# Kernel tuning notes

Hardware: AMD Instinct MI355X
Metric: run time of the kernel (lower is better)

## Reference

```python
import jax, jax.numpy as jnp
import numpy as np

B, S, E, H = 4, 2048, 512, 1024

def setup_inputs() -> dict:
    key = jax.random.key(0)
    ks = jax.random.split(key, 8)
    s = 1.0 / np.sqrt(H)
    return {
        "hidden_states": jax.random.normal(ks[0], (B, S, H), jnp.float32),
        "external_embeddings": jax.random.normal(ks[1], (B, E, H), jnp.float32),
        "Wq": jax.random.normal(ks[2], (H, H), jnp.float32) * s,
        "bq": jax.random.normal(ks[3], (H,), jnp.float32) * 0.02,
        "Wk": jax.random.normal(ks[4], (H, H), jnp.float32) * s,
        "bk": jax.random.normal(ks[5], (H,), jnp.float32) * 0.02,
        "Wv": jax.random.normal(ks[6], (H, H), jnp.float32) * s,
        "bv": jax.random.normal(ks[7], (H,), jnp.float32) * 0.02,
    }

def reference(hidden_states, external_embeddings, Wq, bq, Wk, bk, Wv, bv):
    # Projections (torch Linear semantics: here weights stored as [in,out])
    q = hidden_states @ Wq + bq              # [B,S,H]
    k_tok = hidden_states @ Wk + bk          # [B,S,H]
    v_tok = hidden_states @ Wv + bv          # [B,S,H]
    k_ext = external_embeddings @ Wk + bk    # [B,E,H]
    v_ext = external_embeddings @ Wv + bv    # [B,E,H]
    # Each token attends to [its own key] ++ [external keys]; NO 1/sqrt(d) scaling
    # and NO head splitting, matching the original forward exactly.
    s_self = jnp.einsum('bsh,bsh->bs', q, k_tok)[..., None]   # [B,S,1]
    s_ext = jnp.einsum('bsh,beh->bse', q, k_ext)              # [B,S,E]
    scores = jnp.concatenate([s_self, s_ext], axis=-1)        # [B,S,1+E]
    probs = jax.nn.softmax(scores, axis=-1)
    ctx = probs[..., :1] * v_tok + jnp.einsum('bse,beh->bsh', probs[..., 1:], v_ext)
    return ctx  # [B,S,H]
```

## Files before the change

kernel.cpp:

```cpp
#include <hip/hip_runtime.h>
#include <stdint.h>

#define BB 4
#define SS 2048
#define EE 512
#define HH 1024

typedef _Float16 f16;
typedef __attribute__((ext_vector_type(8))) _Float16 f16x8;
typedef __attribute__((ext_vector_type(4))) _Float16 f16x4;
typedef __attribute__((ext_vector_type(4))) float f32x4;

__device__ __forceinline__ void async16(void* lds, const void* g) {
  __builtin_amdgcn_global_load_lds(
      (const __attribute__((address_space(1))) unsigned int*)g,
      (__attribute__((address_space(3))) unsigned int*)lds, 16, 0, 0);
}

#define MFMA16 __builtin_amdgcn_mfma_f32_16x16x32_f16

template <int TERMS>
__device__ __forceinline__ void gemm_core(
    const f16* Ah, const f16* Al, const f16* Bh, const f16* Bl, int K, int ld,
    f16* lAh, f16* lAl, f16* lBh, f16* lBl, f32x4 acc[4][4]) {
  const int tid = threadIdx.x;
  const int wave = tid >> 6;
  const int lane = tid & 63;
  const int lrow = lane >> 2;
  const int lcol = (((lane & 3) ^ ((lane >> 3) & 3))) * 8;
  const int waveM = (wave >> 1) * 64;
  const int waveN = (wave & 1) * 64;
  const int frow = lane & 15;
  const int fk = ((lane >> 4) ^ ((frow >> 1) & 3)) * 8;

  for (int k0 = 0; k0 < K; k0 += 32) {
    __syncthreads();
#pragma unroll
    for (int i = 0; i < 2; ++i) {
      const int r0 = (wave * 2 + i) * 16;
      const size_t goff = (size_t)(r0 + lrow) * ld + (k0 + lcol);
      async16(&lAh[r0 * 32], Ah + goff);
      async16(&lBh[r0 * 32], Bh + goff);
      if (TERMS >= 2) async16(&lBl[r0 * 32], Bl + goff);
      if (TERMS >= 3) async16(&lAl[r0 * 32], Al + goff);
    }
    __syncthreads();

    f16x8 a[4], bh[4], bl[4], al[4];
#pragma unroll
    for (int i = 0; i < 4; ++i) {
      a[i] = *(const f16x8*)&lAh[(waveM + i * 16 + frow) * 32 + fk];
      bh[i] = *(const f16x8*)&lBh[(waveN + i * 16 + frow) * 32 + fk];
      if (TERMS >= 2) bl[i] = *(const f16x8*)&lBl[(waveN + i * 16 + frow) * 32 + fk];
      if (TERMS >= 3) al[i] = *(const f16x8*)&lAl[(waveM + i * 16 + frow) * 32 + fk];
    }
#pragma unroll
    for (int i = 0; i < 4; ++i)
#pragma unroll
      for (int j = 0; j < 4; ++j) {
        acc[i][j] = MFMA16(a[i], bh[j], acc[i][j], 0, 0, 0);
        if (TERMS >= 2)
          acc[i][j] = MFMA16(a[i], bl[j], acc[i][j], 0, 0, 0);
        if (TERMS >= 3)
          acc[i][j] = MFMA16(al[i], bh[j], acc[i][j], 0, 0, 0);
      }
  }
}

__global__ __launch_bounds__(256) void cast_kernel(const float* __restrict__ xh32,
                                                   const float* __restrict__ xe32,
                                                   f16* __restrict__ xh,
                                                   f16* __restrict__ xe) {
  const int i = blockIdx.x * 256 + threadIdx.x;
  const int n4h = 8192 * HH / 4;
  const float* src = i < n4h ? xh32 : xe32;
  f16* dst = i < n4h ? xh : xe;
  const int k = i < n4h ? i : i - n4h;
  const float4 v = ((const float4*)src)[k];
  f16x4 o;
  o.x = (f16)v.x; o.y = (f16)v.y; o.z = (f16)v.z; o.w = (f16)v.w;
  ((f16x4*)dst)[k] = o;
}

__global__ void wsplit_kernel(const float* __restrict__ Wq, const float* __restrict__ Wk,
                              const float* __restrict__ Wv, f16* __restrict__ wt_hi,
                              f16* __restrict__ wt_lo) {
  __shared__ float tile[32][33];
  const int k0 = blockIdx.x * 32;
  const int n0g = blockIdx.y * 32;
  const int which = n0g >> 10;
  const float* W = which == 0 ? Wq : (which == 1 ? Wk : Wv);
  const int n0 = n0g & 1023;
  const int tx = threadIdx.x, ty = threadIdx.y;
#pragma unroll
  for (int i = 0; i < 32; i += 8)
    tile[ty + i][tx] = W[(size_t)(k0 + ty + i) * 1024 + n0 + tx];
  __syncthreads();
#pragma unroll
  for (int i = 0; i < 32; i += 8) {
    const int np = n0g + ty + i;
    const float v = tile[tx][ty + i];
    const size_t idx = (size_t)np * 1024 + k0 + tx;
    const f16 h = (f16)v;
    wt_hi[idx] = h;
    wt_lo[idx] = (f16)(v - (float)h);
  }
}

__global__ __launch_bounds__(512, 2) void proj_kernel(
    const f16* __restrict__ xh, const f16* __restrict__ xe,
    const f16* __restrict__ wt_hi, const f16* __restrict__ wt_lo,
    const float* __restrict__ bq, const float* __restrict__ bk,
    const float* __restrict__ bv, f16* __restrict__ q_hi, f16* __restrict__ q_lo,
    f16* __restrict__ kt, f16* __restrict__ vt,
    f16* __restrict__ ke_hi, f16* __restrict__ ke_lo, f16* __restrict__ veT) {
  const int g = blockIdx.x;
  const int j = g & 7;
  const int s = g >> 3;
  int mrow0, colB0;
  bool ext = false, splitB = false;
  if (s < 20) {
    splitB = true;
    if (s < 16) {
      colB0 = (s >> 2) * 256;
      mrow0 = ((s & 3) * 8 + j) * 256;
    } else {
      ext = true;
      colB0 = 1024 + (s - 16) * 256;
      mrow0 = j * 256;
    }
  } else {
    const int s2 = s - 20;
    if (s2 < 32) {
      colB0 = (4 + (s2 >> 2)) * 256;
      mrow0 = ((s2 & 3) * 8 + j) * 256;
    } else {
      ext = true;
      colB0 = 1024 + (4 + (s2 - 32)) * 256;
      mrow0 = j * 256;
    }
  }
  const int NT = splitB ? 32 : 16;

  __shared__ f16 lds[65536];

  const int tid = threadIdx.x;
  const int wave = tid >> 6, lane = tid & 63;
  const int wm = wave >> 2, wn = wave & 3;
  const int frow = lane & 15, qd = lane >> 4;

  const f16* A0 = (ext ? xe : xh) + (size_t)mrow0 * HH;
  const f16* Bhi = wt_hi + (size_t)colB0 * HH;
  const f16* Blo = wt_lo + (size_t)colB0 * HH;

  const int srow = tid >> 2;
  const int scol = ((tid & 3) ^ ((srow >> 1) & 3)) * 8;
  const size_t gO0 = (size_t)srow * HH + scol;
  const size_t gO1 = (size_t)(128 + srow) * HH + scol;
  const int ldst0 = (wave * 64) * 8;
  const int ldst1 = (512 + wave * 64) * 8;

  int offA[8], offB[4];
#pragma unroll
  for (int i = 0; i < 8; ++i) {
    const int r = wm * 128 + i * 16 + frow;
    offA[i] = r * 32 + ((qd ^ ((r >> 1) & 3)) * 8);
  }
#pragma unroll
  for (int jj = 0; jj < 4; ++jj) {
    const int r = wn * 64 + jj * 16 + frow;
    offB[jj] = r * 32 + ((qd ^ ((r >> 1) & 3)) * 8);
  }

  f32x4 acc[8][4];
#pragma unroll
  for (int i = 0; i < 8; ++i)
#pragma unroll
    for (int jj = 0; jj < 4; ++jj)
#pragma unroll
      for (int r = 0; r < 4; ++r) acc[i][jj][r] = 0.0f;

  {
    f16* dA0 = &lds[0];
    f16* dB0 = &lds[32768];
    f16* dA1 = &lds[8192];
    f16* dB1 = &lds[32768 + 8192];
    async16(&dA0[ldst0], A0 + gO0);       async16(&dA0[ldst1], A0 + gO1);
    async16(&dB0[ldst0], Bhi + gO0);      async16(&dB0[ldst1], Bhi + gO1);
    async16(&dA1[ldst0], A0 + 32 + gO0);  async16(&dA1[ldst1], A0 + 32 + gO1);
    async16(&dB1[ldst0], Bhi + 32 + gO0); async16(&dB1[ldst1], Bhi + 32 + gO1);
  }
  asm volatile("s_waitcnt vmcnt(4)" ::: "memory");
  __builtin_amdgcn_s_barrier();

  for (int t = 0; t < NT; ++t) {
    const int cur = t & 1, nxt = cur ^ 1;
    const bool st = (t + 1 < NT);
    const int kn = ((t + 1) & 15) * 64;
    const f16* An = A0 + kn;
    const f16* Bn = (((t + 1) & 16) ? Blo : Bhi) + kn;
    const f16* lA0 = &lds[(cur * 2 + 0) * 8192];
    const f16* lB0 = &lds[32768 + (cur * 2 + 0) * 8192];
    const f16* lA1 = &lds[(cur * 2 + 1) * 8192];
    const f16* lB1 = &lds[32768 + (cur * 2 + 1) * 8192];
    f16* sA0 = &lds[(nxt * 2 + 0) * 8192];
    f16* sB0 = &lds[32768 + (nxt * 2 + 0) * 8192];
    f16* sA1 = &lds[(nxt * 2 + 1) * 8192];
    f16* sB1 = &lds[32768 + (nxt * 2 + 1) * 8192];

    f16x8 a[8], b0, b1;

#pragma unroll
    for (int i = 0; i < 8; ++i) a[i] = *(const f16x8*)&lA0[offA[i]];
    b0 = *(const f16x8*)&lB0[offB[0]];
    b1 = *(const f16x8*)&lB0[offB[1]];
    if (st) { async16(&sA0[ldst0], An + gO0); async16(&sA0[ldst1], An + gO1); }
    __builtin_amdgcn_s_barrier();
    __builtin_amdgcn_s_setprio(1);
#pragma unroll
    for (int i = 0; i < 8; ++i) {
      acc[i][0] = MFMA16(a[i], b0, acc[i][0], 0, 0, 0);
      acc[i][1] = MFMA16(a[i], b1, acc[i][1], 0, 0, 0);
    }
    __builtin_amdgcn_s_setprio(0);
    __builtin_amdgcn_s_barrier();

    b0 = *(const f16x8*)&lB0[offB[2]];
    b1 = *(const f16x8*)&lB0[offB[3]];
    if (st) { async16(&sB0[ldst0], Bn + gO0); async16(&sB0[ldst1], Bn + gO1); }
    __builtin_amdgcn_s_barrier();
    __builtin_amdgcn_s_setprio(1);
#pragma unroll
    for (int i = 0; i < 8; ++i) {
      acc[i][2] = MFMA16(a[i], b0, acc[i][2], 0, 0, 0);
      acc[i][3] = MFMA16(a[i], b1, acc[i][3], 0, 0, 0);
    }
    __builtin_amdgcn_s_setprio(0);
    if (t == NT - 1) {
      asm volatile("s_waitcnt vmcnt(0)" ::: "memory");
    } else {
      asm volatile("s_waitcnt vmcnt(4)" ::: "memory");
    }
    __builtin_amdgcn_s_barrier();

#pragma unroll
    for (int i = 0; i < 8; ++i) a[i] = *(const f16x8*)&lA1[offA[i]];
    b0 = *(const f16x8*)&lB1[offB[0]];
    b1 = *(const f16x8*)&lB1[offB[1]];
    if (st) { async16(&sA1[ldst0], An + 32 + gO0); async16(&sA1[ldst1], An + 32 + gO1); }
    __builtin_amdgcn_s_barrier();
    __builtin_amdgcn_s_setprio(1);
#pragma unroll
    for (int i = 0; i < 8; ++i) {
      acc[i][0] = MFMA16(a[i], b0, acc[i][0], 0, 0, 0);
      acc[i][1] = MFMA16(a[i], b1, acc[i][1], 0, 0, 0);
    }
    __builtin_amdgcn_s_setprio(0);
    __builtin_amdgcn_s_barrier();

    b0 = *(const f16x8*)&lB1[offB[2]];
    b1 = *(const f16x8*)&lB1[offB[3]];
    if (st) { async16(&sB1[ldst0], Bn + 32 + gO0); async16(&sB1[ldst1], Bn + 32 + gO1); }
    __builtin_amdgcn_s_barrier();
    __builtin_amdgcn_s_setprio(1);
#pragma unroll
    for (int i = 0; i < 8; ++i) {
      acc[i][2] = MFMA16(a[i], b0, acc[i][2], 0, 0, 0);
      acc[i][3] = MFMA16(a[i], b1, acc[i][3], 0, 0, 0);
    }
    __builtin_amdgcn_s_setprio(0);
    asm volatile("s_waitcnt vmcnt(4)" ::: "memory");
    __builtin_amdgcn_s_barrier();
  }

  const int er0 = wm * 128 + qd * 4;
  const int ec0 = wn * 64 + frow;
  float bias[4];
#pragma unroll
  for (int jj = 0; jj < 4; ++jj) {
    const int c = colB0 + ec0 + jj * 16;
    bias[jj] = c < 1024 ? bq[c] : (c < 2048 ? bk[c - 1024] : bv[c - 2048]);
  }

  if (!ext) {
    if (colB0 < 1024) {
#pragma unroll
      for (int jj = 0; jj < 4; ++jj) {
        const int c = colB0 + ec0 + jj * 16;
#pragma unroll
        for (int i = 0; i < 8; ++i)
#pragma unroll
          for (int r = 0; r < 4; ++r) {
            const int row = mrow0 + er0 + i * 16 + r;
            const float val = acc[i][jj][r] + bias[jj];
            const size_t idx = (size_t)row * HH + c;
            const f16 h = (f16)val;
            q_hi[idx] = h;
            q_lo[idx] = (f16)(val - (float)h);
          }
      }
    } else if (colB0 < 2048) {
#pragma unroll
      for (int jj = 0; jj < 4; ++jj) {
        const int c = colB0 + ec0 + jj * 16 - 1024;
#pragma unroll
        for (int i = 0; i < 8; ++i)
#pragma unroll
          for (int r = 0; r < 4; ++r) {
            const int row = mrow0 + er0 + i * 16 + r;
            kt[(size_t)row * HH + c] = (f16)(acc[i][jj][r] + bias[jj]);
          }
      }
    } else {
#pragma unroll
      for (int jj = 0; jj < 4; ++jj) {
        const int c = colB0 + ec0 + jj * 16 - 2048;
#pragma unroll
        for (int i = 0; i < 8; ++i)
#pragma unroll
          for (int r = 0; r < 4; ++r) {
            const int row = mrow0 + er0 + i * 16 + r;
            vt[(size_t)row * HH + c] = (f16)(acc[i][jj][r] + bias[jj]);
          }
      }
    }
  } else {
    if (colB0 < 2048) {
#pragma unroll
      for (int jj = 0; jj < 4; ++jj) {
        const int c = colB0 + ec0 + jj * 16 - 1024;
#pragma unroll
        for (int i = 0; i < 8; ++i)
#pragma unroll
          for (int r = 0; r < 4; ++r) {
            const int row = mrow0 + er0 + i * 16 + r;
            const float val = acc[i][jj][r] + bias[jj];
            const size_t idx = (size_t)row * HH + c;
            const f16 h = (f16)val;
            ke_hi[idx] = h;
            ke_lo[idx] = (f16)(val - (float)h);
          }
      }
    } else {
      f16* tl = lds;
      const int b = mrow0 >> 9, e0 = mrow0 & 511;
      const int h0 = colB0 - 2048;
#pragma unroll
      for (int p = 0; p < 2; ++p) {
        __syncthreads();
        if ((wn >> 1) == p) {
          const int hL = (wn & 1) * 64 + frow;
#pragma unroll
          for (int jj = 0; jj < 4; ++jj)
#pragma unroll
            for (int i = 0; i < 8; ++i)
#pragma unroll
              for (int r = 0; r < 4; ++r) {
                const int e = er0 + i * 16 + r;
                tl[(hL + jj * 16) * 264 + e] = (f16)(acc[i][jj][r] + bias[jj]);
              }
        }
        __syncthreads();
        for (int c = tid; c < 128 * 32; c += 512) {
          const int hL = c >> 5, ch = c & 31;
          const f16x8 v = *(const f16x8*)&tl[hL * 264 + ch * 8];
          *(f16x8*)&veT[(size_t)(b * HH + h0 + p * 128 + hL) * EE + e0 + ch * 8] = v;
        }
      }
    }
  }
}

__global__ __launch_bounds__(256, 4) void score_kernel(
    const f16* __restrict__ q_hi, const f16* __restrict__ q_lo,
    const f16* __restrict__ ke_hi, const f16* __restrict__ ke_lo,
    float* __restrict__ s_part) {
  const int b = blockIdx.z & 3;
  const int khalf = blockIdx.z >> 2;
  const int mtile = blockIdx.y;
  const int ntile = blockIdx.x;
  __shared__ f16 lds[4 * 4096];
  const size_t aoff = ((size_t)b * SS + mtile * 128) * HH + khalf * 512;
  const size_t boff = ((size_t)b * EE + ntile * 128) * HH + khalf * 512;

  f32x4 acc[4][4];
#pragma unroll
  for (int i = 0; i < 4; ++i)
#pragma unroll
    for (int j = 0; j < 4; ++j)
#pragma unroll
      for (int r = 0; r < 4; ++r) acc[i][j][r] = 0.0f;

  gemm_core<3>(q_hi + aoff, q_lo + aoff, ke_hi + boff, ke_lo + boff, 512, HH,
               lds, lds + 4096, lds + 8192, lds + 12288, acc);

  float* dst = s_part + (size_t)khalf * BB * SS * EE;
  const int tid = threadIdx.x, wave = tid >> 6, lane = tid & 63;
  const int waveM = (wave >> 1) * 64, waveN = (wave & 1) * 64;
  const int colIn16 = lane & 15, rowQuad = (lane >> 4) * 4;
#pragma unroll
  for (int j = 0; j < 4; ++j) {
    const int e = ntile * 128 + waveN + j * 16 + colIn16;
#pragma unroll
    for (int i = 0; i < 4; ++i)
#pragma unroll
      for (int r = 0; r < 4; ++r) {
        const int s = mtile * 128 + waveM + i * 16 + rowQuad + r;
        dst[((size_t)b * SS + s) * EE + e] = acc[i][j][r];
      }
  }
}

__global__ __launch_bounds__(256) void softmax_kernel(
    const f16* __restrict__ q_hi, const f16* __restrict__ q_lo,
    const f16* __restrict__ kt, const float* __restrict__ s_part,
    f16* __restrict__ probs, float* __restrict__ p_self) {
  const int t = blockIdx.x * 4 + (threadIdx.x >> 6);
  const int lane = threadIdx.x & 63;

  const size_t base = (size_t)t * HH;
  float ss = 0.f;
#pragma unroll
  for (int it = 0; it < 4; ++it) {
    const int off = it * 256 + lane * 4;
    const f16x4 qh = *(const f16x4*)&q_hi[base + off];
    const f16x4 ql = *(const f16x4*)&q_lo[base + off];
    const f16x4 kh = *(const f16x4*)&kt[base + off];
    ss += ((float)qh.x + (float)ql.x) * (float)kh.x;
    ss += ((float)qh.y + (float)ql.y) * (float)kh.y;
    ss += ((float)qh.z + (float)ql.z) * (float)kh.z;
    ss += ((float)qh.w + (float)ql.w) * (float)kh.w;
  }
#pragma unroll
  for (int m = 32; m > 0; m >>= 1) ss += __shfl_xor(ss, m, 64);

  const float* r0 = s_part + (size_t)t * EE;
  const float* r1 = s_part + (size_t)BB * SS * EE + (size_t)t * EE;
  const float4 a0 = *(const float4*)&r0[lane * 4];
  const float4 a1 = *(const float4*)&r0[256 + lane * 4];
  const float4 c0 = *(const float4*)&r1[lane * 4];
  const float4 c1 = *(const float4*)&r1[256 + lane * 4];
  const float v0x = a0.x + c0.x, v0y = a0.y + c0.y, v0z = a0.z + c0.z, v0w = a0.w + c0.w;
  const float v1x = a1.x + c1.x, v1y = a1.y + c1.y, v1z = a1.z + c1.z, v1w = a1.w + c1.w;
  float m = fmaxf(fmaxf(fmaxf(v0x, v0y), fmaxf(v0z, v0w)),
                  fmaxf(fmaxf(v1x, v1y), fmaxf(v1z, v1w)));
#pragma unroll
  for (int sh = 32; sh > 0; sh >>= 1) m = fmaxf(m, __shfl_xor(m, sh, 64));
  m = fmaxf(m, ss);
  const float e0 = __expf(v0x - m), e1 = __expf(v0y - m);
  const float e2 = __expf(v0z - m), e3 = __expf(v0w - m);
  const float e4 = __expf(v1x - m), e5 = __expf(v1y - m);
  const float e6 = __expf(v1z - m), e7 = __expf(v1w - m);
  float sum = ((e0 + e1) + (e2 + e3)) + ((e4 + e5) + (e6 + e7));
#pragma unroll
  for (int sh = 32; sh > 0; sh >>= 1) sum += __shfl_xor(sum, sh, 64);
  const float es = __expf(ss - m);
  const float inv = 1.0f / (sum + es);
  f16x4 p0, p1;
  p0.x = (f16)(e0 * inv); p0.y = (f16)(e1 * inv);
  p0.z = (f16)(e2 * inv); p0.w = (f16)(e3 * inv);
  p1.x = (f16)(e4 * inv); p1.y = (f16)(e5 * inv);
  p1.z = (f16)(e6 * inv); p1.w = (f16)(e7 * inv);
  *(f16x4*)&probs[(size_t)t * EE + lane * 4] = p0;
  *(f16x4*)&probs[(size_t)t * EE + 256 + lane * 4] = p1;
  if (lane == 0) p_self[t] = es * inv;
}

__global__ __launch_bounds__(256, 4) void pv_kernel(
    const f16* __restrict__ probs, const f16* __restrict__ veT,
    const float* __restrict__ p_self, const f16* __restrict__ vt,
    float* __restrict__ out) {
  const int b = blockIdx.z;
  const int mtile = blockIdx.y;
  const int ntile = blockIdx.x;
  __shared__ f16 lds[2 * 4096];
  const size_t aoff = ((size_t)b * SS + mtile * 128) * EE;
  const size_t boff = ((size_t)b * HH + ntile * 128) * EE;

  f32x4 acc[4][4];
#pragma unroll
  for (int i = 0; i < 4; ++i)
#pragma unroll
    for (int j = 0; j < 4; ++j)
#pragma unroll
      for (int r = 0; r < 4; ++r) acc[i][j][r] = 0.0f;

  gemm_core<1>(probs + aoff, nullptr, veT + boff, nullptr, EE, EE,
               lds, nullptr, lds + 4096, nullptr, acc);

  const int tid = threadIdx.x, wave = tid >> 6, lane = tid & 63;
  const int waveM = (wave >> 1) * 64, waveN = (wave & 1) * 64;
  const int colIn16 = lane & 15, rowQuad = (lane >> 4) * 4;
#pragma unroll
  for (int j = 0; j < 4; ++j) {
    const int h = ntile * 128 + waveN + j * 16 + colIn16;
#pragma unroll
    for (int i = 0; i < 4; ++i)
#pragma unroll
      for (int r = 0; r < 4; ++r) {
        const int s = mtile * 128 + waveM + i * 16 + rowQuad + r;
        const size_t t = (size_t)b * SS + s;
        __builtin_nontemporal_store(
            acc[i][j][r] + p_self[t] * (float)vt[t * HH + h], &out[t * HH + h]);
      }
  }
}

extern "C" void kernel_launch(void* const* d_in, const int* in_sizes, int n_in,
                              void* d_out, int out_size, void* d_ws, size_t ws_size,
                              hipStream_t stream) {
  const float* hidden = (const float*)d_in[0];
  const float* ext    = (const float*)d_in[1];
  const float* Wq = (const float*)d_in[2];
  const float* bq = (const float*)d_in[3];
  const float* Wk = (const float*)d_in[4];
  const float* bk = (const float*)d_in[5];
  const float* Wv = (const float*)d_in[6];
  const float* bv = (const float*)d_in[7];
  float* out = (float*)d_out;

  char* ws = (char*)d_ws;
  size_t off = 0;
  auto alloc = [&](size_t bytes) {
    char* p = ws + off;
    off += (bytes + 255) & ~(size_t)255;
    return p;
  };
  const size_t TOK = 8192, EXT = 2048;
  f16* xh    = (f16*)alloc(TOK * HH * 2);
  f16* xe    = (f16*)alloc(EXT * HH * 2);
  f16* wt_hi = (f16*)alloc(3072ull * HH * 2);
  f16* wt_lo = (f16*)alloc(3072ull * HH * 2);
  f16* q_hi  = (f16*)alloc(TOK * HH * 2);
  f16* q_lo  = (f16*)alloc(TOK * HH * 2);
  f16* kt    = (f16*)alloc(TOK * HH * 2);
  f16* vt    = (f16*)alloc(TOK * HH * 2);
  f16* ke_hi = (f16*)alloc(EXT * HH * 2);
  f16* ke_lo = (f16*)alloc(EXT * HH * 2);
  f16* veT   = (f16*)alloc((size_t)BB * HH * EE * 2);
  float* p_self = (float*)alloc(TOK * 4);
  float* s_part = (float*)alloc(2ull * BB * SS * EE * 4);
  f16* probs    = (f16*)alloc((size_t)BB * SS * EE * 2);

  cast_kernel<<<10240, 256, 0, stream>>>(hidden, ext, xh, xe);
  wsplit_kernel<<<dim3(32, 96), dim3(32, 8), 0, stream>>>(Wq, Wk, Wv, wt_hi, wt_lo);

  proj_kernel<<<448, 512, 0, stream>>>(
      xh, xe, wt_hi, wt_lo, bq, bk, bv,
      q_hi, q_lo, kt, vt, ke_hi, ke_lo, veT);

  score_kernel<<<dim3(4, 16, 8), 256, 0, stream>>>(q_hi, q_lo, ke_hi, ke_lo, s_part);
  softmax_kernel<<<2048, 256, 0, stream>>>(q_hi, q_lo, kt, s_part, probs, p_self);
  pv_kernel<<<dim3(8, 16, 4), 256, 0, stream>>>(probs, veT, p_self, vt, out);
}
```

Measured before the change: 306.1 us.

## Pipeline score and PV GEMMs with multi-buffered LDS and larger 256-row tiles

Replaces the shared single-buffered gemm_core in score_kernel and pv_kernel with custom pipelines. Score uses double-buffered LDS and pv uses triple-buffered LDS, with async global-to-LDS loads for the next K slice interleaved between MFMA phases under explicit vmcnt waits and s_setprio. Blocks grow to 512 threads covering 256x128 output tiles, so each B tile is reused across more rows. The goal is to hide load latency behind MFMA work and cut barrier stalls, at the cost of more LDS per block, fewer blocks, and fragile hand-counted wait counts.

```diff
diff --git a/kernel.cpp b/kernel.cpp
--- a/kernel.cpp
+++ b/kernel.cpp
@@ -18,54 +18,6 @@
 }
 
 #define MFMA16 __builtin_amdgcn_mfma_f32_16x16x32_f16
-
-template <int TERMS>
-__device__ __forceinline__ void gemm_core(
-    const f16* Ah, const f16* Al, const f16* Bh, const f16* Bl, int K, int ld,
-    f16* lAh, f16* lAl, f16* lBh, f16* lBl, f32x4 acc[4][4]) {
-  const int tid = threadIdx.x;
-  const int wave = tid >> 6;
-  const int lane = tid & 63;
-  const int lrow = lane >> 2;
-  const int lcol = (((lane & 3) ^ ((lane >> 3) & 3))) * 8;
-  const int waveM = (wave >> 1) * 64;
-  const int waveN = (wave & 1) * 64;
-  const int frow = lane & 15;
-  const int fk = ((lane >> 4) ^ ((frow >> 1) & 3)) * 8;
-
-  for (int k0 = 0; k0 < K; k0 += 32) {
-    __syncthreads();
-#pragma unroll
-    for (int i = 0; i < 2; ++i) {
-      const int r0 = (wave * 2 + i) * 16;
-      const size_t goff = (size_t)(r0 + lrow) * ld + (k0 + lcol);
-      async16(&lAh[r0 * 32], Ah + goff);
-      async16(&lBh[r0 * 32], Bh + goff);
-      if (TERMS >= 2) async16(&lBl[r0 * 32], Bl + goff);
-      if (TERMS >= 3) async16(&lAl[r0 * 32], Al + goff);
-    }
-    __syncthreads();
-
-    f16x8 a[4], bh[4], bl[4], al[4];
-#pragma unroll
-    for (int i = 0; i < 4; ++i) {
-      a[i] = *(const f16x8*)&lAh[(waveM + i * 16 + frow) * 32 + fk];
-      bh[i] = *(const f16x8*)&lBh[(waveN + i * 16 + frow) * 32 + fk];
-      if (TERMS >= 2) bl[i] = *(const f16x8*)&lBl[(waveN + i * 16 + frow) * 32 + fk];
-      if (TERMS >= 3) al[i] = *(const f16x8*)&lAl[(waveM + i * 16 + frow) * 32 + fk];
-    }
-#pragma unroll
-    for (int i = 0; i < 4; ++i)
-#pragma unroll
-      for (int j = 0; j < 4; ++j) {
-        acc[i][j] = MFMA16(a[i], bh[j], acc[i][j], 0, 0, 0);
-        if (TERMS >= 2)
-          acc[i][j] = MFMA16(a[i], bl[j], acc[i][j], 0, 0, 0);
-        if (TERMS >= 3)
-          acc[i][j] = MFMA16(al[i], bh[j], acc[i][j], 0, 0, 0);
-      }
-  }
-}
 
 __global__ __launch_bounds__(256) void cast_kernel(const float* __restrict__ xh32,
                                                    const float* __restrict__ xe32,
@@ -371,7 +323,7 @@
   }
 }
 
-__global__ __launch_bounds__(256, 4) void score_kernel(
+__global__ __launch_bounds__(512, 2) void score_kernel(
     const f16* __restrict__ q_hi, const f16* __restrict__ q_lo,
     const f16* __restrict__ ke_hi, const f16* __restrict__ ke_lo,
     float* __restrict__ s_part) {
@@ -379,34 +331,137 @@
   const int khalf = blockIdx.z >> 2;
   const int mtile = blockIdx.y;
   const int ntile = blockIdx.x;
-  __shared__ f16 lds[4 * 4096];
-  const size_t aoff = ((size_t)b * SS + mtile * 128) * HH + khalf * 512;
+
+  __shared__ f16 lds[49152];
+
+  const int tid = threadIdx.x;
+  const int wave = tid >> 6, lane = tid & 63;
+  const int wm = wave >> 1, wn = wave & 1;
+  const int frow = lane & 15, qd = lane >> 4;
+
+  const size_t aoff = ((size_t)b * SS + mtile * 256) * HH + khalf * 512;
   const size_t boff = ((size_t)b * EE + ntile * 128) * HH + khalf * 512;
+  const f16* Ah = q_hi + aoff;
+  const f16* Al = q_lo + aoff;
+  const f16* Bh = ke_hi + boff;
+  const f16* Bl = ke_lo + boff;
+
+  const int srow = tid >> 2;
+  const int scol = ((tid & 3) ^ ((srow >> 1) & 3)) * 8;
+  const size_t gA0 = (size_t)srow * HH + scol;
+  const size_t gA1 = (size_t)(128 + srow) * HH + scol;
+  const int ldstA0 = (wave * 64) * 8;
+  const int ldstA1 = (512 + wave * 64) * 8;
+  const int ldstB0 = (wave * 64) * 8;
+
+  int offA[4], offB[4];
+#pragma unroll
+  for (int i = 0; i < 4; ++i) {
+    const int r = wm * 64 + i * 16 + frow;
+    offA[i] = r * 32 + ((qd ^ ((r >> 1) & 3)) * 8);
+  }
+#pragma unroll
+  for (int jj = 0; jj < 4; ++jj) {
+    const int r = wn * 64 + jj * 16 + frow;
+    offB[jj] = r * 32 + ((qd ^ ((r >> 1) & 3)) * 8);
+  }
 
   f32x4 acc[4][4];
 #pragma unroll
   for (int i = 0; i < 4; ++i)
 #pragma unroll
-    for (int j = 0; j < 4; ++j)
-#pragma unroll
-      for (int r = 0; r < 4; ++r) acc[i][j][r] = 0.0f;
-
-  gemm_core<3>(q_hi + aoff, q_lo + aoff, ke_hi + boff, ke_lo + boff, 512, HH,
-               lds, lds + 4096, lds + 8192, lds + 12288, acc);
-
-  float* dst = s_part + (size_t)khalf * BB * SS * EE;
-  const int tid = threadIdx.x, wave = tid >> 6, lane = tid & 63;
-  const int waveM = (wave >> 1) * 64, waveN = (wave & 1) * 64;
-  const int colIn16 = lane & 15, rowQuad = (lane >> 4) * 4;
-#pragma unroll
-  for (int j = 0; j < 4; ++j) {
-    const int e = ntile * 128 + waveN + j * 16 + colIn16;
+    for (int jj = 0; jj < 4; ++jj)
+#pragma unroll
+      for (int r = 0; r < 4; ++r) acc[i][jj][r] = 0.0f;
+
+  {
+    f16* dAh = &lds[0];
+    f16* dAl = &lds[8192];
+    f16* dBh = &lds[16384];
+    f16* dBl = &lds[20480];
+    async16(&dAh[ldstA0], Ah + gA0); async16(&dAh[ldstA1], Ah + gA1);
+    async16(&dBh[ldstB0], Bh + gA0);
+    async16(&dBl[ldstB0], Bl + gA0);
+    async16(&dAl[ldstA0], Al + gA0); async16(&dAl[ldstA1], Al + gA1);
+  }
+  asm volatile("s_waitcnt vmcnt(3)" ::: "memory");
+  __builtin_amdgcn_s_barrier();
+
+  for (int t = 0; t < 16; ++t) {
+    const int cur = t & 1, nxt = cur ^ 1;
+    const bool st = (t < 15);
+    const int kk = (t + 1) * 32;
+    const f16* lAh = &lds[cur * 24576];
+    const f16* lAl = &lds[cur * 24576 + 8192];
+    const f16* lBh = &lds[cur * 24576 + 16384];
+    const f16* lBl = &lds[cur * 24576 + 20480];
+    f16* sAh = &lds[nxt * 24576];
+    f16* sAl = &lds[nxt * 24576 + 8192];
+    f16* sBh = &lds[nxt * 24576 + 16384];
+    f16* sBl = &lds[nxt * 24576 + 20480];
+
+    f16x8 ah[4], bh[4], x[4];
+
+#pragma unroll
+    for (int i = 0; i < 4; ++i) ah[i] = *(const f16x8*)&lAh[offA[i]];
+#pragma unroll
+    for (int jj = 0; jj < 4; ++jj) bh[jj] = *(const f16x8*)&lBh[offB[jj]];
+    if (st) {
+      async16(&sAh[ldstA0], Ah + kk + gA0); async16(&sAh[ldstA1], Ah + kk + gA1);
+      async16(&sBh[ldstB0], Bh + kk + gA0);
+    }
+    __builtin_amdgcn_s_barrier();
+    __builtin_amdgcn_s_setprio(1);
 #pragma unroll
     for (int i = 0; i < 4; ++i)
 #pragma unroll
+      for (int jj = 0; jj < 4; ++jj)
+        acc[i][jj] = MFMA16(ah[i], bh[jj], acc[i][jj], 0, 0, 0);
+    __builtin_amdgcn_s_setprio(0);
+    if (st) { asm volatile("s_waitcnt vmcnt(5)" ::: "memory"); }
+    else    { asm volatile("s_waitcnt vmcnt(2)" ::: "memory"); }
+    __builtin_amdgcn_s_barrier();
+
+#pragma unroll
+    for (int jj = 0; jj < 4; ++jj) x[jj] = *(const f16x8*)&lBl[offB[jj]];
+    if (st) async16(&sBl[ldstB0], Bl + kk + gA0);
+    __builtin_amdgcn_s_barrier();
+    __builtin_amdgcn_s_setprio(1);
+#pragma unroll
+    for (int i = 0; i < 4; ++i)
+#pragma unroll
+      for (int jj = 0; jj < 4; ++jj)
+        acc[i][jj] = MFMA16(ah[i], x[jj], acc[i][jj], 0, 0, 0);
+    __builtin_amdgcn_s_setprio(0);
+    if (st) { asm volatile("s_waitcnt vmcnt(4)" ::: "memory"); }
+    else    { asm volatile("s_waitcnt vmcnt(0)" ::: "memory"); }
+    __builtin_amdgcn_s_barrier();
+
+#pragma unroll
+    for (int i = 0; i < 4; ++i) x[i] = *(const f16x8*)&lAl[offA[i]];
+    if (st) { async16(&sAl[ldstA0], Al + kk + gA0); async16(&sAl[ldstA1], Al + kk + gA1); }
+    __builtin_amdgcn_s_barrier();
+    __builtin_amdgcn_s_setprio(1);
+#pragma unroll
+    for (int i = 0; i < 4; ++i)
+#pragma unroll
+      for (int jj = 0; jj < 4; ++jj)
+        acc[i][jj] = MFMA16(x[i], bh[jj], acc[i][jj], 0, 0, 0);
+    __builtin_amdgcn_s_setprio(0);
+    if (st) { asm volatile("s_waitcnt vmcnt(3)" ::: "memory"); }
+    __builtin_amdgcn_s_barrier();
+  }
+
+  float* dst = s_part + (size_t)khalf * BB * SS * EE + (size_t)b * SS * EE;
+#pragma unroll
+  for (int jj = 0; jj < 4; ++jj) {
+    const int e = ntile * 128 + wn * 64 + jj * 16 + frow;
+#pragma unroll
+    for (int i = 0; i < 4; ++i)
+#pragma unroll
       for (int r = 0; r < 4; ++r) {
-        const int s = mtile * 128 + waveM + i * 16 + rowQuad + r;
-        dst[((size_t)b * SS + s) * EE + e] = acc[i][j][r];
+        const int s = mtile * 256 + wm * 64 + i * 16 + qd * 4 + r;
+        dst[(size_t)s * EE + e] = acc[i][jj][r];
       }
   }
 }
@@ -466,42 +521,121 @@
   if (lane == 0) p_self[t] = es * inv;
 }
 
-__global__ __launch_bounds__(256, 4) void pv_kernel(
+__global__ __launch_bounds__(512, 2) void pv_kernel(
     const f16* __restrict__ probs, const f16* __restrict__ veT,
     const float* __restrict__ p_self, const f16* __restrict__ vt,
     float* __restrict__ out) {
   const int b = blockIdx.z;
   const int mtile = blockIdx.y;
   const int ntile = blockIdx.x;
-  __shared__ f16 lds[2 * 4096];
-  const size_t aoff = ((size_t)b * SS + mtile * 128) * EE;
+
+  __shared__ f16 lds[36864];
+
+  const int tid = threadIdx.x;
+  const int wave = tid >> 6, lane = tid & 63;
+  const int wm = wave >> 1, wn = wave & 1;
+  const int frow = lane & 15, qd = lane >> 4;
+
+  const size_t aoff = ((size_t)b * SS + mtile * 256) * EE;
   const size_t boff = ((size_t)b * HH + ntile * 128) * EE;
+  const f16* A = probs + aoff;
+  const f16* Bv = veT + boff;
+
+  const int srow = tid >> 2;
+  const int scol = ((tid & 3) ^ ((srow >> 1) & 3)) * 8;
+  const size_t gA0 = (size_t)srow * EE + scol;
+  const size_t gA1 = (size_t)(128 + srow) * EE + scol;
+  const int ldstA0 = (wave * 64) * 8;
+  const int ldstA1 = (512 + wave * 64) * 8;
+  const int ldstB0 = (wave * 64) * 8;
+
+  int offA[4], offB[4];
+#pragma unroll
+  for (int i = 0; i < 4; ++i) {
+    const int r = wm * 64 + i * 16 + frow;
+    offA[i] = r * 32 + ((qd ^ ((r >> 1) & 3)) * 8);
+  }
+#pragma unroll
+  for (int jj = 0; jj < 4; ++jj) {
+    const int r = wn * 64 + jj * 16 + frow;
+    offB[jj] = r * 32 + ((qd ^ ((r >> 1) & 3)) * 8);
+  }
 
   f32x4 acc[4][4];
 #pragma unroll
   for (int i = 0; i < 4; ++i)
 #pragma unroll
-    for (int j = 0; j < 4; ++j)
-#pragma unroll
-      for (int r = 0; r < 4; ++r) acc[i][j][r] = 0.0f;
-
-  gemm_core<1>(probs + aoff, nullptr, veT + boff, nullptr, EE, EE,
-               lds, nullptr, lds + 4096, nullptr, acc);
-
-  const int tid = threadIdx.x, wave = tid >> 6, lane = tid & 63;
-  const int waveM = (wave >> 1) * 64, waveN = (wave & 1) * 64;
-  const int colIn16 = lane & 15, rowQuad = (lane >> 4) * 4;
-#pragma unroll
-  for (int j = 0; j < 4; ++j) {
-    const int h = ntile * 128 + waveN + j * 16 + colIn16;
+    for (int jj = 0; jj < 4; ++jj)
+#pragma unroll
+      for (int r = 0; r < 4; ++r) acc[i][jj][r] = 0.0f;
+
+  {
+    f16* dA0 = &lds[0], *dB0 = &lds[8192];
+    f16* dA1 = &lds[12288], *dB1 = &lds[12288 + 8192];
+    async16(&dA0[ldstA0], A + gA0); async16(&dA0[ldstA1], A + gA1);
+    async16(&dB0[ldstB0], Bv + gA0);
+    async16(&dA1[ldstA0], A + 32 + gA0); async16(&dA1[ldstA1], A + 32 + gA1);
+    async16(&dB1[ldstB0], Bv + 32 + gA0);
+  }
+  asm volatile("s_waitcnt vmcnt(3)" ::: "memory");
+  __builtin_amdgcn_s_barrier();
+
+  int cur = 0, stg = 2;
+  for (int t = 0; t < 16; ++t) {
+    const bool st = (t < 14);
+    const int kk = (t + 2) * 32;
+    const f16* lA = &lds[cur * 12288];
+    const f16* lB = &lds[cur * 12288 + 8192];
+    f16* sA = &lds[stg * 12288];
+    f16* sB = &lds[stg * 12288 + 8192];
+
+    f16x8 a[4], b[4];
+
+#pragma unroll
+    for (int i = 0; i < 4; ++i) a[i] = *(const f16x8*)&lA[offA[i]];
+    b[0] = *(const f16x8*)&lB[offB[0]];
+    b[1] = *(const f16x8*)&lB[offB[1]];
+    if (st) { async16(&sA[ldstA0], A + kk + gA0); async16(&sA[ldstA1], A + kk + gA1); }
+    __builtin_amdgcn_s_barrier();
+    __builtin_amdgcn_s_setprio(1);
+#pragma unroll
+    for (int i = 0; i < 4; ++i) {
+      acc[i][0] = MFMA16(a[i], b[0], acc[i][0], 0, 0, 0);
+      acc[i][1] = MFMA16(a[i], b[1], acc[i][1], 0, 0, 0);
+    }
+    __builtin_amdgcn_s_setprio(0);
+    __builtin_amdgcn_s_barrier();
+
+    b[2] = *(const f16x8*)&lB[offB[2]];
+    b[3] = *(const f16x8*)&lB[offB[3]];
+    if (st) async16(&sB[ldstB0], Bv + kk + gA0);
+    __builtin_amdgcn_s_barrier();
+    __builtin_amdgcn_s_setprio(1);
+#pragma unroll
+    for (int i = 0; i < 4; ++i) {
+      acc[i][2] = MFMA16(a[i], b[2], acc[i][2], 0, 0, 0);
+      acc[i][3] = MFMA16(a[i], b[3], acc[i][3], 0, 0, 0);
+    }
+    __builtin_amdgcn_s_setprio(0);
+    if (t < 14)      { asm volatile("s_waitcnt vmcnt(3)" ::: "memory"); }
+    else if (t == 14){ asm volatile("s_waitcnt vmcnt(0)" ::: "memory"); }
+    __builtin_amdgcn_s_barrier();
+
+    cur = (cur == 2) ? 0 : cur + 1;
+    stg = (stg == 2) ? 0 : stg + 1;
+  }
+
+#pragma unroll
+  for (int jj = 0; jj < 4; ++jj) {
+    const int h = ntile * 128 + wn * 64 + jj * 16 + frow;
 #pragma unroll
     for (int i = 0; i < 4; ++i)
 #pragma unroll
       for (int r = 0; r < 4; ++r) {
-        const int s = mtile * 128 + waveM + i * 16 + rowQuad + r;
+        const int s = mtile * 256 + wm * 64 + i * 16 + qd * 4 + r;
         const size_t t = (size_t)b * SS + s;
         __builtin_nontemporal_store(
-            acc[i][j][r] + p_self[t] * (float)vt[t * HH + h], &out[t * HH + h]);
+            acc[i][jj][r] + p_self[t] * (float)vt[t * HH + h], &out[t * HH + h]);
       }
   }
 }
@@ -549,7 +683,7 @@
       xh, xe, wt_hi, wt_lo, bq, bk, bv,
       q_hi, q_lo, kt, vt, ke_hi, ke_lo, veT);
 
-  score_kernel<<<dim3(4, 16, 8), 256, 0, stream>>>(q_hi, q_lo, ke_hi, ke_lo, s_part);
+  score_kernel<<<dim3(4, 8, 8), 512, 0, stream>>>(q_hi, q_lo, ke_hi, ke_lo, s_part);
   softmax_kernel<<<2048, 256, 0, stream>>>(q_hi, q_lo, kt, s_part, probs, p_self);
-  pv_kernel<<<dim3(8, 16, 4), 256, 0, stream>>>(probs, veT, p_self, vt, out);
-}
+  pv_kernel<<<dim3(8, 8, 4), 512, 0, stream>>>(probs, veT, p_self, vt, out);
+}
```

After: 281.1 us. 8.1% less time.
